# Performance work log

Measured on AMD Instinct MI355X. Metric: run time of the kernel, lower is better.

## Reference

```python
import jax, jax.numpy as jnp
import numpy as np

N = 512          # num_satellites
STATE_DIM = 6    # pos(3) + vel(3)
OBJ_DIM = 58
F = STATE_DIM + OBJ_DIM          # node feature dim = 64
HID = (128, 64, 32)
EDGE_IN = 2 * F + 1              # sender + receiver + distance
NODE_IN = F + HID[-1]            # node feats + aggregated messages


def _linear_init(key, d_in, d_out):
    kw, _ = jax.random.split(key)
    w = jax.random.normal(kw, (d_in, d_out), jnp.float32) / np.sqrt(d_in).astype(np.float32)
    b = jnp.zeros((d_out,), jnp.float32)
    return w, b


def setup_inputs() -> dict:
    key = jax.random.key(0)
    ks = jax.random.split(key, 12)
    ew0, eb0 = _linear_init(ks[0], EDGE_IN, HID[0])
    ew1, eb1 = _linear_init(ks[1], HID[0], HID[1])
    ew2, eb2 = _linear_init(ks[2], HID[1], HID[2])
    nw0, nb0 = _linear_init(ks[3], NODE_IN, HID[0])
    nw1, nb1 = _linear_init(ks[4], HID[0], HID[1])
    nw2, nb2 = _linear_init(ks[5], HID[1], HID[2])
    nwo, nbo = _linear_init(ks[6], HID[2], F)   # residual projection back to F
    rw, rb = _linear_init(ks[7], F, 3)          # control readout
    states = jax.random.normal(ks[8], (N, STATE_DIM), jnp.float32)
    objectives = jax.random.normal(ks[9], (OBJ_DIM,), jnp.float32)
    return dict(states=states, objectives=objectives,
                ew0=ew0, eb0=eb0, ew1=ew1, eb1=eb1, ew2=ew2, eb2=eb2,
                nw0=nw0, nb0=nb0, nw1=nw1, nb1=nb1, nw2=nw2, nb2=nb2,
                nwo=nwo, nbo=nbo, rw=rw, rb=rb,
                num_message_passing=3)


def _edge_index(n):
    ii, jj = np.meshgrid(np.arange(n), np.arange(n), indexing='ij')
    m = ii != jj
    return jnp.asarray(ii[m]), jnp.asarray(jj[m])  # sender i, receiver j; E = n*(n-1)


def reference(states, objectives, ew0, eb0, ew1, eb1, ew2, eb2,
              nw0, nb0, nw1, nb1, nw2, nb2, nwo, nbo, rw, rb,
              num_message_passing):
    n = states.shape[0]
    snd, rcv = _edge_index(n)
    # node features: state concat broadcast objectives -> [N, F]
    nf = jnp.concatenate(
        [states, jnp.broadcast_to(objectives, (n, objectives.shape[0]))], axis=-1)
    # distances from raw states (constant across iterations): [E, 1]
    rel = states[rcv, :3] - states[snd, :3]
    dist = jnp.linalg.norm(rel, axis=-1, keepdims=True)
    relu = jax.nn.relu
    for _ in range(num_message_passing):
        # edge MLP over all E edges: [E, 2F+1] -> [E, 32]
        x = jnp.concatenate([nf[snd], nf[rcv], dist], axis=-1)
        h = relu(x @ ew0 + eb0)
        h = relu(h @ ew1 + eb1)
        msg = relu(h @ ew2 + eb2)
        # sum-aggregate incoming messages at receiver j: [N, 32]
        agg = jax.ops.segment_sum(msg, rcv, num_segments=n)
        # node MLP + residual: [N, F+32] -> [N, F]
        y = jnp.concatenate([nf, agg], axis=-1)
        h = relu(y @ nw0 + nb0)
        h = relu(h @ nw1 + nb1)
        h = relu(h @ nw2 + nb2)
        nf = nf + h @ nwo + nbo
    # control readout: [N, 3]
    return nf @ rw + rb
```

## Files before the change

### kernel.cpp

```cpp
#include <hip/hip_runtime.h>
#include <math.h>

#define NSAT 512
#define FDIM 64
#define H0D  128
#define H1D  64
#define H2D  32
#define KP1  68

#define WS_NF    0
#define WS_PRES  (WS_NF   + NSAT * FDIM)
#define WS_PRER  (WS_PRES + NSAT * H0D)
#define WS_AGG   (WS_PRER + NSAT * H0D)
#define WS_WT    (WS_AGG  + 4 * NSAT * H2D)

using short8_t = __attribute__((ext_vector_type(8))) short;
using short4_t = __attribute__((ext_vector_type(4))) short;
using int4_t   = __attribute__((ext_vector_type(4))) int;
using int2_t   = __attribute__((ext_vector_type(2))) int;
using floatx4  = __attribute__((ext_vector_type(4))) float;
using floatx16 = __attribute__((ext_vector_type(16))) float;

__device__ __forceinline__ void split_ru(float x, short& hi, short& lo) {
    unsigned u = __builtin_bit_cast(unsigned, x);
    unsigned hb = (u + 0x8000u) >> 16;
    hi = (short)hb;
    float r = x - __builtin_bit_cast(float, hb << 16);
    lo = (short)((__builtin_bit_cast(unsigned, r) + 0x8000u) >> 16);
}

__device__ __forceinline__ void split8_pk(const float* __restrict__ v,
                                          short8_t& bh, short8_t& bl) {
    unsigned t[8]; unsigned ru[8];
    #pragma unroll
    for (int e = 0; e < 8; ++e) {
        unsigned u = __builtin_bit_cast(unsigned, v[e]);
        t[e] = u + 0x8000u;
        float r = v[e] - __builtin_bit_cast(float, t[e] & 0xffff0000u);
        ru[e] = __builtin_bit_cast(unsigned, r);
    }
    int4_t hv, lv;
    #pragma unroll
    for (int p = 0; p < 4; ++p) {
        hv[p] = (int)__builtin_amdgcn_perm(t[2*p+1],  t[2*p],  0x07060302u);
        lv[p] = (int)__builtin_amdgcn_perm(ru[2*p+1], ru[2*p], 0x07060302u);
    }
    bh = __builtin_bit_cast(short8_t, hv);
    bl = __builtin_bit_cast(short8_t, lv);
}

__device__ __forceinline__ void split4_pk(const float* __restrict__ v,
                                          short4_t& h, short4_t& l) {
    unsigned t[4]; unsigned ru[4];
    #pragma unroll
    for (int e = 0; e < 4; ++e) {
        unsigned u = __builtin_bit_cast(unsigned, v[e]);
        t[e] = u + 0x8000u;
        float r = v[e] - __builtin_bit_cast(float, t[e] & 0xffff0000u);
        ru[e] = __builtin_bit_cast(unsigned, r);
    }
    int2_t hv, lv;
    #pragma unroll
    for (int p = 0; p < 2; ++p) {
        hv[p] = (int)__builtin_amdgcn_perm(t[2*p+1],  t[2*p],  0x07060302u);
        lv[p] = (int)__builtin_amdgcn_perm(ru[2*p+1], ru[2*p], 0x07060302u);
    }
    h = __builtin_bit_cast(short4_t, hv);
    l = __builtin_bit_cast(short4_t, lv);
}

__device__ __forceinline__ float dot8(const float* __restrict__ x,
                                      const float* __restrict__ w,
                                      int n, int stride, int col, float bias) {
    float s[8] = {bias, 0.f, 0.f, 0.f, 0.f, 0.f, 0.f, 0.f};
    #pragma unroll
    for (int f = 0; f < 8; ++f) {
        for (int q = f; q < n; q += 8)
            ;
    }
    return s[0];
}

__device__ __forceinline__ void compute_pre(const float* __restrict__ nfl,
                                            const float* __restrict__ ew0,
                                            const float* __restrict__ eb0,
                                            int i, int t,
                                            float* __restrict__ preSA,
                                            float* __restrict__ preR) {
    if (t < H0D) {
        int k = t;
        float s[8] = {0.f, 0.f, 0.f, 0.f, 0.f, 0.f, 0.f, 0.f};
        #pragma unroll
        for (int f = 0; f < FDIM; f += 8) {
            #pragma unroll
            for (int e = 0; e < 8; ++e)
                s[e] = fmaf(nfl[f + e], ew0[(f + e) * H0D + k], s[e]);
        }
        float r = ((s[0] + s[1]) + (s[2] + s[3])) + ((s[4] + s[5]) + (s[6] + s[7]));
        int kk = (k >> 3) & 7, lhi = k >> 6, j = k & 7;
        preSA[((i >> 5) * 8 + kk) * 512 + (lhi * 32 + (i & 31)) * 8 + j] = r;
    } else {
        int k = t - H0D;
        float s[8] = {eb0[k], 0.f, 0.f, 0.f, 0.f, 0.f, 0.f, 0.f};
        #pragma unroll
        for (int f = 0; f < FDIM; f += 8) {
            #pragma unroll
            for (int e = 0; e < 8; ++e)
                s[e] = fmaf(nfl[f + e], ew0[(FDIM + f + e) * H0D + k], s[e]);
        }
        preR[i * H0D + k] =
            ((s[0] + s[1]) + (s[2] + s[3])) + ((s[4] + s[5]) + (s[6] + s[7]));
    }
}

__global__ void setup_kernel(const float* __restrict__ states,
                             const float* __restrict__ objectives,
                             const float* __restrict__ ew0,
                             const float* __restrict__ eb0,
                             const float* __restrict__ ew1,
                             const float* __restrict__ ew2,
                             float* __restrict__ nf,
                             float* __restrict__ preSA,
                             float* __restrict__ preR,
                             short* __restrict__ w1A_hi,
                             short* __restrict__ w1A_lo,
                             short* __restrict__ w2t_hi,
                             short* __restrict__ w2t_lo) {
    __shared__ float nfl[FDIM];
    int b = blockIdx.x, t = threadIdx.x;
    if (b < NSAT) {
        if (t < FDIM) {
            float v = (t < 6) ? states[b * 6 + t] : objectives[t - 6];
            nfl[t] = v;
            nf[b * FDIM + t] = v;
        }
        __syncthreads();
        compute_pre(nfl, ew0, eb0, b, t, preSA, preR);
    } else {
        int e = (b - NSAT) * 256 + t;
        if (e < H1D * H0D) {
            int j  = e & 7;
            int l  = (e >> 3) & 63;
            int kk = (e >> 9) & 7;
            int mh = e >> 12;
            int m = mh * 32 + (l & 31);
            int k = (l >> 5) * 64 + kk * 8 + j;
            short hi, lo; split_ru(ew1[k * H1D + m], hi, lo);
            w1A_hi[e] = hi; w1A_lo[e] = lo;
        } else if (e < H1D * H0D + H2D * H1D) {
            int e2 = e - H1D * H0D;
            int c = e2 >> 6, k = e2 & 63;
            short hi, lo; split_ru(ew2[k * H2D + c], hi, lo);
            w2t_hi[e2] = hi; w2t_lo[e2] = lo;
        }
    }
}

__global__ __launch_bounds__(256)
void edge_agg_kernel(const float* __restrict__ states,
                     const float* __restrict__ preSA,
                     const float* __restrict__ preR,
                     const float* __restrict__ ew0,
                     const float* __restrict__ eb1,
                     const float* __restrict__ eb2,
                     const short* __restrict__ w1A_hi,
                     const short* __restrict__ w1A_lo,
                     const short* __restrict__ w2t_hi,
                     const short* __restrict__ w2t_lo,
                     float* __restrict__ aggP) {
    __shared__ __align__(16) short h1_hi[128 * KP1];
    __shared__ __align__(16) short h1_lo[128 * KP1];
    __shared__ __align__(16) float preR_l[H0D];
    __shared__ __align__(16) float wd_l[H0D];
    __shared__ __align__(16) float eb1_l[H1D];
    __shared__ float eb2_l[H2D];
    __shared__ __align__(16) float red_l[4 * H2D];

    int t = threadIdx.x, b = blockIdx.x;
    int j = b >> 2, g = b & 3;
    int w = t >> 6, lane = t & 63;
    int lhi = lane >> 5, llo = lane & 31;

    if (t < H0D) preR_l[t] = preR[j * H0D + t];
    else         wd_l[t - H0D] = ew0[H0D * H0D + (t - H0D)];
    if (t < 64)      eb1_l[t] = eb1[t];
    else if (t < 96) eb2_l[t - 64] = eb2[t - 64];
    __syncthreads();

    int s_loc = w * 32 + llo;
    int s_glb = g * 128 + s_loc;
    float dx = states[s_glb * 6 + 0] - states[j * 6 + 0];
    float dy = states[s_glb * 6 + 1] - states[j * 6 + 1];
    float dz = states[s_glb * 6 + 2] - states[j * 6 + 2];
    float d = sqrtf(dx * dx + dy * dy + dz * dz);

    const float* pS = preSA + (size_t)((g * 4 + w) * 8) * 512 + lane * 8;
    const short* pAh0 = w1A_hi + lane * 8;
    const short* pAl0 = w1A_lo + lane * 8;

    floatx16 accA, accB;
    #pragma unroll
    for (int r = 0; r < 16; ++r) { accA[r] = 0.f; accB[r] = 0.f; }

    #pragma unroll
    for (int kk = 0; kk < 8; ++kk) {
        float4 a0 = *(const float4*)(pS + kk * 512);
        float4 a1 = *(const float4*)(pS + kk * 512 + 4);
        int kb = lhi * 64 + kk * 8;
        float4 r0 = *(const float4*)&preR_l[kb];
        float4 r1 = *(const float4*)&preR_l[kb + 4];
        float4 q0 = *(const float4*)&wd_l[kb];
        float4 q1 = *(const float4*)&wd_l[kb + 4];
        float v[8];
        v[0] = fmaxf(a0.x + fmaf(d, q0.x, r0.x), 0.f);
        v[1] = fmaxf(a0.y + fmaf(d, q0.y, r0.y), 0.f);
        v[2] = fmaxf(a0.z + fmaf(d, q0.z, r0.z), 0.f);
        v[3] = fmaxf(a0.w + fmaf(d, q0.w, r0.w), 0.f);
        v[4] = fmaxf(a1.x + fmaf(d, q1.x, r1.x), 0.f);
        v[5] = fmaxf(a1.y + fmaf(d, q1.y, r1.y), 0.f);
        v[6] = fmaxf(a1.z + fmaf(d, q1.z, r1.z), 0.f);
        v[7] = fmaxf(a1.w + fmaf(d, q1.w, r1.w), 0.f);
        short8_t bh, bl;
        split8_pk(v, bh, bl);
        short8_t ah0 = *(const short8_t*)(pAh0 + kk * 512);
        short8_t al0 = *(const short8_t*)(pAl0 + kk * 512);
        short8_t ah1 = *(const short8_t*)(pAh0 + 4096 + kk * 512);
        short8_t al1 = *(const short8_t*)(pAl0 + 4096 + kk * 512);
        accA = __builtin_amdgcn_mfma_f32_32x32x16_bf16(ah0, bh, accA, 0, 0, 0);
        accA = __builtin_amdgcn_mfma_f32_32x32x16_bf16(ah0, bl, accA, 0, 0, 0);
        accA = __builtin_amdgcn_mfma_f32_32x32x16_bf16(al0, bh, accA, 0, 0, 0);
        accB = __builtin_amdgcn_mfma_f32_32x32x16_bf16(ah1, bh, accB, 0, 0, 0);
        accB = __builtin_amdgcn_mfma_f32_32x32x16_bf16(ah1, bl, accB, 0, 0, 0);
        accB = __builtin_amdgcn_mfma_f32_32x32x16_bf16(al1, bh, accB, 0, 0, 0);
    }

    {
        int s1 = s_loc;
        #pragma unroll
        for (int mh = 0; mh < 2; ++mh) {
            #pragma unroll
            for (int q = 0; q < 4; ++q) {
                int m0 = mh * 32 + q * 8 + lhi * 4;
                float vv[4];
                #pragma unroll
                for (int r = 0; r < 4; ++r) {
                    float c = mh ? accB[q * 4 + r] : accA[q * 4 + r];
                    vv[r] = fmaxf(c + eb1_l[m0 + r], 0.f);
                }
                short4_t ph, pl;
                split4_pk(vv, ph, pl);
                *(short4_t*)&h1_hi[s1 * KP1 + m0] = ph;
                *(short4_t*)&h1_lo[s1 * KP1 + m0] = pl;
            }
        }
    }

    int lq = lane >> 4, l15 = lane & 15;
    int sA = w * 32 + l15, sB = sA + 16;
    floatx4 aA0, aA1, aB0, aB1;
    #pragma unroll
    for (int r = 0; r < 4; ++r) { aA0[r]=0.f; aA1[r]=0.f; aB0[r]=0.f; aB1[r]=0.f; }
    const short* pA2h0 = w2t_hi + l15 * H1D + lq * 8;
    const short* pA2l0 = w2t_lo + l15 * H1D + lq * 8;
    const short* pA2h1 = w2t_hi + (16 + l15) * H1D + lq * 8;
    const short* pA2l1 = w2t_lo + (16 + l15) * H1D + lq * 8;
    int boA = sA * KP1 + lq * 8, boB = sB * KP1 + lq * 8;
    #pragma unroll
    for (int kk = 0; kk < 2; ++kk) {
        short4_t b0, b1, c0, c1;
        b0 = *(const short4_t*)&h1_hi[boA + kk * 32];
        b1 = *(const short4_t*)&h1_hi[boA + kk * 32 + 4];
        c0 = *(const short4_t*)&h1_lo[boA + kk * 32];
        c1 = *(const short4_t*)&h1_lo[boA + kk * 32 + 4];
        short8_t bhA = __builtin_shufflevector(b0, b1, 0,1,2,3,4,5,6,7);
        short8_t blA = __builtin_shufflevector(c0, c1, 0,1,2,3,4,5,6,7);
        b0 = *(const short4_t*)&h1_hi[boB + kk * 32];
        b1 = *(const short4_t*)&h1_hi[boB + kk * 32 + 4];
        c0 = *(const short4_t*)&h1_lo[boB + kk * 32];
        c1 = *(const short4_t*)&h1_lo[boB + kk * 32 + 4];
        short8_t bhB = __builtin_shufflevector(b0, b1, 0,1,2,3,4,5,6,7);
        short8_t blB = __builtin_shufflevector(c0, c1, 0,1,2,3,4,5,6,7);
        short8_t a0h = *(const short8_t*)(pA2h0 + kk * 32);
        short8_t a0l = *(const short8_t*)(pA2l0 + kk * 32);
        short8_t a1h = *(const short8_t*)(pA2h1 + kk * 32);
        short8_t a1l = *(const short8_t*)(pA2l1 + kk * 32);
        aA0 = __builtin_amdgcn_mfma_f32_16x16x32_bf16(a0h, bhA, aA0, 0, 0, 0);
        aA0 = __builtin_amdgcn_mfma_f32_16x16x32_bf16(a0h, blA, aA0, 0, 0, 0);
        aA0 = __builtin_amdgcn_mfma_f32_16x16x32_bf16(a0l, bhA, aA0, 0, 0, 0);
        aA1 = __builtin_amdgcn_mfma_f32_16x16x32_bf16(a1h, bhA, aA1, 0, 0, 0);
        aA1 = __builtin_amdgcn_mfma_f32_16x16x32_bf16(a1h, blA, aA1, 0, 0, 0);
        aA1 = __builtin_amdgcn_mfma_f32_16x16x32_bf16(a1l, bhA, aA1, 0, 0, 0);
        aB0 = __builtin_amdgcn_mfma_f32_16x16x32_bf16(a0h, bhB, aB0, 0, 0, 0);
        aB0 = __builtin_amdgcn_mfma_f32_16x16x32_bf16(a0h, blB, aB0, 0, 0, 0);
        aB0 = __builtin_amdgcn_mfma_f32_16x16x32_bf16(a0l, bhB, aB0, 0, 0, 0);
        aB1 = __builtin_amdgcn_mfma_f32_16x16x32_bf16(a1h, bhB, aB1, 0, 0, 0);
        aB1 = __builtin_amdgcn_mfma_f32_16x16x32_bf16(a1h, blB, aB1, 0, 0, 0);
        aB1 = __builtin_amdgcn_mfma_f32_16x16x32_bf16(a1l, bhB, aB1, 0, 0, 0);
    }

    {
        bool selfA = (g * 128 + sA == j);
        bool selfB = (g * 128 + sB == j);
        float red[8];
        #pragma unroll
        for (int r = 0; r < 4; ++r) {
            float vA = fmaxf(aA0[r] + eb2_l[lq * 4 + r], 0.f);
            float vB = fmaxf(aB0[r] + eb2_l[lq * 4 + r], 0.f);
            if (selfA) vA = 0.f;
            if (selfB) vB = 0.f;
            float v = vA + vB;
            v += __shfl_xor(v, 1, 64); v += __shfl_xor(v, 2, 64);
            v += __shfl_xor(v, 4, 64); v += __shfl_xor(v, 8, 64);
            red[r] = v;
        }
        #pragma unroll
        for (int r = 0; r < 4; ++r) {
            float vA = fmaxf(aA1[r] + eb2_l[16 + lq * 4 + r], 0.f);
            float vB = fmaxf(aB1[r] + eb2_l[16 + lq * 4 + r], 0.f);
            if (selfA) vA = 0.f;
            if (selfB) vB = 0.f;
            float v = vA + vB;
            v += __shfl_xor(v, 1, 64); v += __shfl_xor(v, 2, 64);
            v += __shfl_xor(v, 4, 64); v += __shfl_xor(v, 8, 64);
            red[4 + r] = v;
        }
        if (l15 == 0) {
            *(float4*)&red_l[w * H2D + lq * 4] =
                make_float4(red[0], red[1], red[2], red[3]);
            *(float4*)&red_l[w * H2D + 16 + lq * 4] =
                make_float4(red[4], red[5], red[6], red[7]);
        }
    }
    __syncthreads();
    if (t < H2D) {
        float s = red_l[t] + red_l[H2D + t] + red_l[2*H2D + t] + red_l[3*H2D + t];
        aggP[(g * NSAT + j) * H2D + t] = s;
    }
}

__global__ __launch_bounds__(256)
void node_fused_kernel(const float* __restrict__ aggP,
                       const float* __restrict__ nw0, const float* __restrict__ nb0,
                       const float* __restrict__ nw1, const float* __restrict__ nb1,
                       const float* __restrict__ nw2, const float* __restrict__ nb2,
                       const float* __restrict__ nwo, const float* __restrict__ nbo,
                       const float* __restrict__ ew0, const float* __restrict__ eb0,
                       const float* __restrict__ rw,  const float* __restrict__ rb,
                       float* __restrict__ nf,
                       float* __restrict__ preSA,
                       float* __restrict__ preR,
                       float* __restrict__ out,
                       int final_iter) {
    __shared__ float y[96];
    __shared__ float hA[H0D];
    __shared__ float hB[H1D];
    __shared__ float hC[H2D];
    __shared__ float nfl[FDIM];
    int i = blockIdx.x, t = threadIdx.x;
    if (t < FDIM) y[t] = nf[i * FDIM + t];
    else if (t < 96) {
        int c = t - FDIM;
        float s = 0.f;
        #pragma unroll
        for (int g = 0; g < 4; ++g) s += aggP[(g * NSAT + i) * H2D + c];
        y[t] = s;
    }
    __syncthreads();
    if (t < H0D) {
        float s[8] = {nb0[t], 0.f, 0.f, 0.f, 0.f, 0.f, 0.f, 0.f};
        #pragma unroll
        for (int f = 0; f < 96; f += 8) {
            #pragma unroll
            for (int e = 0; e < 8; ++e)
                s[e] = fmaf(y[f + e], nw0[(f + e) * H0D + t], s[e]);
        }
        hA[t] = fmaxf(((s[0] + s[1]) + (s[2] + s[3])) +
                      ((s[4] + s[5]) + (s[6] + s[7])), 0.f);
    }
    __syncthreads();
    if (t < H1D) {
        float s[8] = {nb1[t], 0.f, 0.f, 0.f, 0.f, 0.f, 0.f, 0.f};
        #pragma unroll
        for (int k = 0; k < H0D; k += 8) {
            #pragma unroll
            for (int e = 0; e < 8; ++e)
                s[e] = fmaf(hA[k + e], nw1[(k + e) * H1D + t], s[e]);
        }
        hB[t] = fmaxf(((s[0] + s[1]) + (s[2] + s[3])) +
                      ((s[4] + s[5]) + (s[6] + s[7])), 0.f);
    }
    __syncthreads();
    if (t < H2D) {
        float s[8] = {nb2[t], 0.f, 0.f, 0.f, 0.f, 0.f, 0.f, 0.f};
        #pragma unroll
        for (int m = 0; m < H1D; m += 8) {
            #pragma unroll
            for (int e = 0; e < 8; ++e)
                s[e] = fmaf(hB[m + e], nw2[(m + e) * H2D + t], s[e]);
        }
        hC[t] = fmaxf(((s[0] + s[1]) + (s[2] + s[3])) +
                      ((s[4] + s[5]) + (s[6] + s[7])), 0.f);
    }
    __syncthreads();
    if (t < FDIM) {
        float s[8] = {nbo[t], 0.f, 0.f, 0.f, 0.f, 0.f, 0.f, 0.f};
        #pragma unroll
        for (int c = 0; c < H2D; c += 8) {
            #pragma unroll
            for (int e = 0; e < 8; ++e)
                s[e] = fmaf(hC[c + e], nwo[(c + e) * FDIM + t], s[e]);
        }
        float v = y[t] + (((s[0] + s[1]) + (s[2] + s[3])) +
                          ((s[4] + s[5]) + (s[6] + s[7])));
        nfl[t] = v;
        if (!final_iter) nf[i * FDIM + t] = v;
    }
    __syncthreads();
    if (final_iter) {
        if (t < 3) {
            float s[8] = {rb[t], 0.f, 0.f, 0.f, 0.f, 0.f, 0.f, 0.f};
            #pragma unroll
            for (int f = 0; f < FDIM; f += 8) {
                #pragma unroll
                for (int e = 0; e < 8; ++e)
                    s[e] = fmaf(nfl[f + e], rw[(f + e) * 3 + t], s[e]);
            }
            out[i * 3 + t] = ((s[0] + s[1]) + (s[2] + s[3])) +
                             ((s[4] + s[5]) + (s[6] + s[7]));
        }
    } else {
        compute_pre(nfl, ew0, eb0, i, t, preSA, preR);
    }
}

extern "C" void kernel_launch(void* const* d_in, const int* in_sizes, int n_in,
                              void* d_out, int out_size, void* d_ws, size_t ws_size,
                              hipStream_t stream) {
    const float* states     = (const float*)d_in[0];
    const float* objectives = (const float*)d_in[1];
    const float* ew0 = (const float*)d_in[2];
    const float* eb0 = (const float*)d_in[3];
    const float* ew1 = (const float*)d_in[4];
    const float* eb1 = (const float*)d_in[5];
    const float* ew2 = (const float*)d_in[6];
    const float* eb2 = (const float*)d_in[7];
    const float* nw0 = (const float*)d_in[8];
    const float* nb0 = (const float*)d_in[9];
    const float* nw1 = (const float*)d_in[10];
    const float* nb1 = (const float*)d_in[11];
    const float* nw2 = (const float*)d_in[12];
    const float* nb2 = (const float*)d_in[13];
    const float* nwo = (const float*)d_in[14];
    const float* nbo = (const float*)d_in[15];
    const float* rw  = (const float*)d_in[16];
    const float* rb  = (const float*)d_in[17];
    float* out = (float*)d_out;
    float* ws  = (float*)d_ws;

    float* nf    = ws + WS_NF;
    float* preSA = ws + WS_PRES;
    float* preR  = ws + WS_PRER;
    float* aggP  = ws + WS_AGG;
    short* w1A_hi = (short*)(ws + WS_WT);
    short* w1A_lo = w1A_hi + H1D * H0D;
    short* w2t_hi = w1A_lo + H1D * H0D;
    short* w2t_lo = w2t_hi + H2D * H1D;

    setup_kernel<<<NSAT + 40, 256, 0, stream>>>(states, objectives, ew0, eb0,
                                                ew1, ew2, nf, preSA, preR,
                                                w1A_hi, w1A_lo, w2t_hi, w2t_lo);
    for (int it = 0; it < 3; ++it) {
        edge_agg_kernel<<<4 * NSAT, 256, 0, stream>>>(states, preSA, preR, ew0,
                                                      eb1, eb2, w1A_hi, w1A_lo,
                                                      w2t_hi, w2t_lo, aggP);
        node_fused_kernel<<<NSAT, 256, 0, stream>>>(aggP, nw0, nb0, nw1, nb1,
                                                    nw2, nb2, nwo, nbo,
                                                    ew0, eb0, rw, rb,
                                                    nf, preSA, preR, out,
                                                    (it == 2) ? 1 : 0);
    }
}
```

Baseline: 183.1 us.

## Halve edge-kernel grid with two sender chunks per block; split node MLP across threads

The edge aggregation kernel now launches two blocks per receiver instead of four, and each block loops over two 128-sender chunks. It accumulates partial sums in a register, which halves the aggP partials the node kernel has to read and sum. The node kernel spreads each small dense layer across all 256 threads by splitting the K dimension, then reduces the partials through shared memory instead of leaving most threads idle. The cost is fewer blocks in the edge kernel, so less parallelism and latency hiding, plus extra barriers per chunk and per layer. A dead helper function is removed.

```diff
diff --git a/kernel.cpp b/kernel.cpp
--- a/kernel.cpp
+++ b/kernel.cpp
@@ -12,7 +12,7 @@
 #define WS_PRES  (WS_NF   + NSAT * FDIM)
 #define WS_PRER  (WS_PRES + NSAT * H0D)
 #define WS_AGG   (WS_PRER + NSAT * H0D)
-#define WS_WT    (WS_AGG  + 4 * NSAT * H2D)
+#define WS_WT    (WS_AGG  + 2 * NSAT * H2D)
 
 using short8_t = __attribute__((ext_vector_type(8))) short;
 using short4_t = __attribute__((ext_vector_type(4))) short;
@@ -67,18 +67,6 @@
     }
     h = __builtin_bit_cast(short4_t, hv);
     l = __builtin_bit_cast(short4_t, lv);
-}
-
-__device__ __forceinline__ float dot8(const float* __restrict__ x,
-                                      const float* __restrict__ w,
-                                      int n, int stride, int col, float bias) {
-    float s[8] = {bias, 0.f, 0.f, 0.f, 0.f, 0.f, 0.f, 0.f};
-    #pragma unroll
-    for (int f = 0; f < 8; ++f) {
-        for (int q = f; q < n; q += 8)
-            ;
-    }
-    return s[0];
 }
 
 __device__ __forceinline__ void compute_pre(const float* __restrict__ nfl,
@@ -177,7 +165,7 @@
     __shared__ __align__(16) float red_l[4 * H2D];
 
     int t = threadIdx.x, b = blockIdx.x;
-    int j = b >> 2, g = b & 3;
+    int j = b >> 1, gg = b & 1;
     int w = t >> 6, lane = t & 63;
     int lhi = lane >> 5, llo = lane & 31;
 
@@ -187,155 +175,162 @@
     else if (t < 96) eb2_l[t - 64] = eb2[t - 64];
     __syncthreads();
 
-    int s_loc = w * 32 + llo;
-    int s_glb = g * 128 + s_loc;
-    float dx = states[s_glb * 6 + 0] - states[j * 6 + 0];
-    float dy = states[s_glb * 6 + 1] - states[j * 6 + 1];
-    float dz = states[s_glb * 6 + 2] - states[j * 6 + 2];
-    float d = sqrtf(dx * dx + dy * dy + dz * dz);
-
-    const float* pS = preSA + (size_t)((g * 4 + w) * 8) * 512 + lane * 8;
-    const short* pAh0 = w1A_hi + lane * 8;
-    const short* pAl0 = w1A_lo + lane * 8;
-
-    floatx16 accA, accB;
-    #pragma unroll
-    for (int r = 0; r < 16; ++r) { accA[r] = 0.f; accB[r] = 0.f; }
-
-    #pragma unroll
-    for (int kk = 0; kk < 8; ++kk) {
-        float4 a0 = *(const float4*)(pS + kk * 512);
-        float4 a1 = *(const float4*)(pS + kk * 512 + 4);
-        int kb = lhi * 64 + kk * 8;
-        float4 r0 = *(const float4*)&preR_l[kb];
-        float4 r1 = *(const float4*)&preR_l[kb + 4];
-        float4 q0 = *(const float4*)&wd_l[kb];
-        float4 q1 = *(const float4*)&wd_l[kb + 4];
-        float v[8];
-        v[0] = fmaxf(a0.x + fmaf(d, q0.x, r0.x), 0.f);
-        v[1] = fmaxf(a0.y + fmaf(d, q0.y, r0.y), 0.f);
-        v[2] = fmaxf(a0.z + fmaf(d, q0.z, r0.z), 0.f);
-        v[3] = fmaxf(a0.w + fmaf(d, q0.w, r0.w), 0.f);
-        v[4] = fmaxf(a1.x + fmaf(d, q1.x, r1.x), 0.f);
-        v[5] = fmaxf(a1.y + fmaf(d, q1.y, r1.y), 0.f);
-        v[6] = fmaxf(a1.z + fmaf(d, q1.z, r1.z), 0.f);
-        v[7] = fmaxf(a1.w + fmaf(d, q1.w, r1.w), 0.f);
-        short8_t bh, bl;
-        split8_pk(v, bh, bl);
-        short8_t ah0 = *(const short8_t*)(pAh0 + kk * 512);
-        short8_t al0 = *(const short8_t*)(pAl0 + kk * 512);
-        short8_t ah1 = *(const short8_t*)(pAh0 + 4096 + kk * 512);
-        short8_t al1 = *(const short8_t*)(pAl0 + 4096 + kk * 512);
-        accA = __builtin_amdgcn_mfma_f32_32x32x16_bf16(ah0, bh, accA, 0, 0, 0);
-        accA = __builtin_amdgcn_mfma_f32_32x32x16_bf16(ah0, bl, accA, 0, 0, 0);
-        accA = __builtin_amdgcn_mfma_f32_32x32x16_bf16(al0, bh, accA, 0, 0, 0);
-        accB = __builtin_amdgcn_mfma_f32_32x32x16_bf16(ah1, bh, accB, 0, 0, 0);
-        accB = __builtin_amdgcn_mfma_f32_32x32x16_bf16(ah1, bl, accB, 0, 0, 0);
-        accB = __builtin_amdgcn_mfma_f32_32x32x16_bf16(al1, bh, accB, 0, 0, 0);
-    }
-
-    {
-        int s1 = s_loc;
-        #pragma unroll
-        for (int mh = 0; mh < 2; ++mh) {
-            #pragma unroll
-            for (int q = 0; q < 4; ++q) {
-                int m0 = mh * 32 + q * 8 + lhi * 4;
-                float vv[4];
+    float jx = states[j * 6 + 0], jy = states[j * 6 + 1], jz = states[j * 6 + 2];
+    int lq = lane >> 4, l15 = lane & 15;
+    float aggLoc = 0.f;
+
+    #pragma unroll 1
+    for (int c = 0; c < 2; ++c) {
+        int s_loc = w * 32 + llo;
+        int s_glb = gg * 256 + c * 128 + s_loc;
+        float dx = states[s_glb * 6 + 0] - jx;
+        float dy = states[s_glb * 6 + 1] - jy;
+        float dz = states[s_glb * 6 + 2] - jz;
+        float d = sqrtf(dx * dx + dy * dy + dz * dz);
+
+        const float* pS = preSA +
+            (size_t)((gg * 8 + c * 4 + w) * 8) * 512 + lane * 8;
+        const short* pAh0 = w1A_hi + lane * 8;
+        const short* pAl0 = w1A_lo + lane * 8;
+
+        floatx16 accA, accB;
+        #pragma unroll
+        for (int r = 0; r < 16; ++r) { accA[r] = 0.f; accB[r] = 0.f; }
+
+        #pragma unroll
+        for (int kk = 0; kk < 8; ++kk) {
+            float4 a0 = *(const float4*)(pS + kk * 512);
+            float4 a1 = *(const float4*)(pS + kk * 512 + 4);
+            int kb = lhi * 64 + kk * 8;
+            float4 r0 = *(const float4*)&preR_l[kb];
+            float4 r1 = *(const float4*)&preR_l[kb + 4];
+            float4 q0 = *(const float4*)&wd_l[kb];
+            float4 q1 = *(const float4*)&wd_l[kb + 4];
+            float v[8];
+            v[0] = fmaxf(a0.x + fmaf(d, q0.x, r0.x), 0.f);
+            v[1] = fmaxf(a0.y + fmaf(d, q0.y, r0.y), 0.f);
+            v[2] = fmaxf(a0.z + fmaf(d, q0.z, r0.z), 0.f);
+            v[3] = fmaxf(a0.w + fmaf(d, q0.w, r0.w), 0.f);
+            v[4] = fmaxf(a1.x + fmaf(d, q1.x, r1.x), 0.f);
+            v[5] = fmaxf(a1.y + fmaf(d, q1.y, r1.y), 0.f);
+            v[6] = fmaxf(a1.z + fmaf(d, q1.z, r1.z), 0.f);
+            v[7] = fmaxf(a1.w + fmaf(d, q1.w, r1.w), 0.f);
+            short8_t bh, bl;
+            split8_pk(v, bh, bl);
+            short8_t ah0 = *(const short8_t*)(pAh0 + kk * 512);
+            short8_t al0 = *(const short8_t*)(pAl0 + kk * 512);
+            short8_t ah1 = *(const short8_t*)(pAh0 + 4096 + kk * 512);
+            short8_t al1 = *(const short8_t*)(pAl0 + 4096 + kk * 512);
+            accA = __builtin_amdgcn_mfma_f32_32x32x16_bf16(ah0, bh, accA, 0, 0, 0);
+            accA = __builtin_amdgcn_mfma_f32_32x32x16_bf16(ah0, bl, accA, 0, 0, 0);
+            accA = __builtin_amdgcn_mfma_f32_32x32x16_bf16(al0, bh, accA, 0, 0, 0);
+            accB = __builtin_amdgcn_mfma_f32_32x32x16_bf16(ah1, bh, accB, 0, 0, 0);
+            accB = __builtin_amdgcn_mfma_f32_32x32x16_bf16(ah1, bl, accB, 0, 0, 0);
+            accB = __builtin_amdgcn_mfma_f32_32x32x16_bf16(al1, bh, accB, 0, 0, 0);
+        }
+
+        {
+            int s1 = s_loc;
+            #pragma unroll
+            for (int mh = 0; mh < 2; ++mh) {
                 #pragma unroll
-                for (int r = 0; r < 4; ++r) {
-                    float c = mh ? accB[q * 4 + r] : accA[q * 4 + r];
-                    vv[r] = fmaxf(c + eb1_l[m0 + r], 0.f);
+                for (int q = 0; q < 4; ++q) {
+                    int m0 = mh * 32 + q * 8 + lhi * 4;
+                    float vv[4];
+                    #pragma unroll
+                    for (int r = 0; r < 4; ++r) {
+                        float cc = mh ? accB[q * 4 + r] : accA[q * 4 + r];
+                        vv[r] = fmaxf(cc + eb1_l[m0 + r], 0.f);
+                    }
+                    short4_t ph, pl;
+                    split4_pk(vv, ph, pl);
+                    *(short4_t*)&h1_hi[s1 * KP1 + m0] = ph;
+                    *(short4_t*)&h1_lo[s1 * KP1 + m0] = pl;
                 }
-                short4_t ph, pl;
-                split4_pk(vv, ph, pl);
-                *(short4_t*)&h1_hi[s1 * KP1 + m0] = ph;
-                *(short4_t*)&h1_lo[s1 * KP1 + m0] = pl;
             }
         }
-    }
-
-    int lq = lane >> 4, l15 = lane & 15;
-    int sA = w * 32 + l15, sB = sA + 16;
-    floatx4 aA0, aA1, aB0, aB1;
-    #pragma unroll
-    for (int r = 0; r < 4; ++r) { aA0[r]=0.f; aA1[r]=0.f; aB0[r]=0.f; aB1[r]=0.f; }
-    const short* pA2h0 = w2t_hi + l15 * H1D + lq * 8;
-    const short* pA2l0 = w2t_lo + l15 * H1D + lq * 8;
-    const short* pA2h1 = w2t_hi + (16 + l15) * H1D + lq * 8;
-    const short* pA2l1 = w2t_lo + (16 + l15) * H1D + lq * 8;
-    int boA = sA * KP1 + lq * 8, boB = sB * KP1 + lq * 8;
-    #pragma unroll
-    for (int kk = 0; kk < 2; ++kk) {
-        short4_t b0, b1, c0, c1;
-        b0 = *(const short4_t*)&h1_hi[boA + kk * 32];
-        b1 = *(const short4_t*)&h1_hi[boA + kk * 32 + 4];
-        c0 = *(const short4_t*)&h1_lo[boA + kk * 32];
-        c1 = *(const short4_t*)&h1_lo[boA + kk * 32 + 4];
-        short8_t bhA = __builtin_shufflevector(b0, b1, 0,1,2,3,4,5,6,7);
-        short8_t blA = __builtin_shufflevector(c0, c1, 0,1,2,3,4,5,6,7);
-        b0 = *(const short4_t*)&h1_hi[boB + kk * 32];
-        b1 = *(const short4_t*)&h1_hi[boB + kk * 32 + 4];
-        c0 = *(const short4_t*)&h1_lo[boB + kk * 32];
-        c1 = *(const short4_t*)&h1_lo[boB + kk * 32 + 4];
-        short8_t bhB = __builtin_shufflevector(b0, b1, 0,1,2,3,4,5,6,7);
-        short8_t blB = __builtin_shufflevector(c0, c1, 0,1,2,3,4,5,6,7);
-        short8_t a0h = *(const short8_t*)(pA2h0 + kk * 32);
-        short8_t a0l = *(const short8_t*)(pA2l0 + kk * 32);
-        short8_t a1h = *(const short8_t*)(pA2h1 + kk * 32);
-        short8_t a1l = *(const short8_t*)(pA2l1 + kk * 32);
-        aA0 = __builtin_amdgcn_mfma_f32_16x16x32_bf16(a0h, bhA, aA0, 0, 0, 0);
-        aA0 = __builtin_amdgcn_mfma_f32_16x16x32_bf16(a0h, blA, aA0, 0, 0, 0);
-        aA0 = __builtin_amdgcn_mfma_f32_16x16x32_bf16(a0l, bhA, aA0, 0, 0, 0);
-        aA1 = __builtin_amdgcn_mfma_f32_16x16x32_bf16(a1h, bhA, aA1, 0, 0, 0);
-        aA1 = __builtin_amdgcn_mfma_f32_16x16x32_bf16(a1h, blA, aA1, 0, 0, 0);
-        aA1 = __builtin_amdgcn_mfma_f32_16x16x32_bf16(a1l, bhA, aA1, 0, 0, 0);
-        aB0 = __builtin_amdgcn_mfma_f32_16x16x32_bf16(a0h, bhB, aB0, 0, 0, 0);
-        aB0 = __builtin_amdgcn_mfma_f32_16x16x32_bf16(a0h, blB, aB0, 0, 0, 0);
-        aB0 = __builtin_amdgcn_mfma_f32_16x16x32_bf16(a0l, bhB, aB0, 0, 0, 0);
-        aB1 = __builtin_amdgcn_mfma_f32_16x16x32_bf16(a1h, bhB, aB1, 0, 0, 0);
-        aB1 = __builtin_amdgcn_mfma_f32_16x16x32_bf16(a1h, blB, aB1, 0, 0, 0);
-        aB1 = __builtin_amdgcn_mfma_f32_16x16x32_bf16(a1l, bhB, aB1, 0, 0, 0);
-    }
-
-    {
-        bool selfA = (g * 128 + sA == j);
-        bool selfB = (g * 128 + sB == j);
-        float red[8];
-        #pragma unroll
-        for (int r = 0; r < 4; ++r) {
-            float vA = fmaxf(aA0[r] + eb2_l[lq * 4 + r], 0.f);
-            float vB = fmaxf(aB0[r] + eb2_l[lq * 4 + r], 0.f);
-            if (selfA) vA = 0.f;
-            if (selfB) vB = 0.f;
-            float v = vA + vB;
-            v += __shfl_xor(v, 1, 64); v += __shfl_xor(v, 2, 64);
-            v += __shfl_xor(v, 4, 64); v += __shfl_xor(v, 8, 64);
-            red[r] = v;
-        }
-        #pragma unroll
-        for (int r = 0; r < 4; ++r) {
-            float vA = fmaxf(aA1[r] + eb2_l[16 + lq * 4 + r], 0.f);
-            float vB = fmaxf(aB1[r] + eb2_l[16 + lq * 4 + r], 0.f);
-            if (selfA) vA = 0.f;
-            if (selfB) vB = 0.f;
-            float v = vA + vB;
-            v += __shfl_xor(v, 1, 64); v += __shfl_xor(v, 2, 64);
-            v += __shfl_xor(v, 4, 64); v += __shfl_xor(v, 8, 64);
-            red[4 + r] = v;
-        }
-        if (l15 == 0) {
-            *(float4*)&red_l[w * H2D + lq * 4] =
-                make_float4(red[0], red[1], red[2], red[3]);
-            *(float4*)&red_l[w * H2D + 16 + lq * 4] =
-                make_float4(red[4], red[5], red[6], red[7]);
-        }
-    }
-    __syncthreads();
-    if (t < H2D) {
-        float s = red_l[t] + red_l[H2D + t] + red_l[2*H2D + t] + red_l[3*H2D + t];
-        aggP[(g * NSAT + j) * H2D + t] = s;
-    }
+
+        int sA = w * 32 + l15, sB = sA + 16;
+        floatx4 aA0, aA1, aB0, aB1;
+        #pragma unroll
+        for (int r = 0; r < 4; ++r) { aA0[r]=0.f; aA1[r]=0.f; aB0[r]=0.f; aB1[r]=0.f; }
+        const short* pA2h0 = w2t_hi + l15 * H1D + lq * 8;
+        const short* pA2l0 = w2t_lo + l15 * H1D + lq * 8;
+        const short* pA2h1 = w2t_hi + (16 + l15) * H1D + lq * 8;
+        const short* pA2l1 = w2t_lo + (16 + l15) * H1D + lq * 8;
+        int boA = sA * KP1 + lq * 8, boB = sB * KP1 + lq * 8;
+        #pragma unroll
+        for (int kk = 0; kk < 2; ++kk) {
+            short4_t b0, b1, c0, c1;
+            b0 = *(const short4_t*)&h1_hi[boA + kk * 32];
+            b1 = *(const short4_t*)&h1_hi[boA + kk * 32 + 4];
+            c0 = *(const short4_t*)&h1_lo[boA + kk * 32];
+            c1 = *(const short4_t*)&h1_lo[boA + kk * 32 + 4];
+            short8_t bhA = __builtin_shufflevector(b0, b1, 0,1,2,3,4,5,6,7);
+            short8_t blA = __builtin_shufflevector(c0, c1, 0,1,2,3,4,5,6,7);
+            b0 = *(const short4_t*)&h1_hi[boB + kk * 32];
+            b1 = *(const short4_t*)&h1_hi[boB + kk * 32 + 4];
+            c0 = *(const short4_t*)&h1_lo[boB + kk * 32];
+            c1 = *(const short4_t*)&h1_lo[boB + kk * 32 + 4];
+            short8_t bhB = __builtin_shufflevector(b0, b1, 0,1,2,3,4,5,6,7);
+            short8_t blB = __builtin_shufflevector(c0, c1, 0,1,2,3,4,5,6,7);
+            short8_t a0h = *(const short8_t*)(pA2h0 + kk * 32);
+            short8_t a0l = *(const short8_t*)(pA2l0 + kk * 32);
+            short8_t a1h = *(const short8_t*)(pA2h1 + kk * 32);
+            short8_t a1l = *(const short8_t*)(pA2l1 + kk * 32);
+            aA0 = __builtin_amdgcn_mfma_f32_16x16x32_bf16(a0h, bhA, aA0, 0, 0, 0);
+            aA0 = __builtin_amdgcn_mfma_f32_16x16x32_bf16(a0h, blA, aA0, 0, 0, 0);
+            aA0 = __builtin_amdgcn_mfma_f32_16x16x32_bf16(a0l, bhA, aA0, 0, 0, 0);
+            aA1 = __builtin_amdgcn_mfma_f32_16x16x32_bf16(a1h, bhA, aA1, 0, 0, 0);
+            aA1 = __builtin_amdgcn_mfma_f32_16x16x32_bf16(a1h, blA, aA1, 0, 0, 0);
+            aA1 = __builtin_amdgcn_mfma_f32_16x16x32_bf16(a1l, bhA, aA1, 0, 0, 0);
+            aB0 = __builtin_amdgcn_mfma_f32_16x16x32_bf16(a0h, bhB, aB0, 0, 0, 0);
+            aB0 = __builtin_amdgcn_mfma_f32_16x16x32_bf16(a0h, blB, aB0, 0, 0, 0);
+            aB0 = __builtin_amdgcn_mfma_f32_16x16x32_bf16(a0l, bhB, aB0, 0, 0, 0);
+            aB1 = __builtin_amdgcn_mfma_f32_16x16x32_bf16(a1h, bhB, aB1, 0, 0, 0);
+            aB1 = __builtin_amdgcn_mfma_f32_16x16x32_bf16(a1h, blB, aB1, 0, 0, 0);
+            aB1 = __builtin_amdgcn_mfma_f32_16x16x32_bf16(a1l, bhB, aB1, 0, 0, 0);
+        }
+
+        {
+            bool selfA = (gg * 256 + c * 128 + sA == j);
+            bool selfB = (gg * 256 + c * 128 + sB == j);
+            float red[8];
+            #pragma unroll
+            for (int r = 0; r < 4; ++r) {
+                float vA = fmaxf(aA0[r] + eb2_l[lq * 4 + r], 0.f);
+                float vB = fmaxf(aB0[r] + eb2_l[lq * 4 + r], 0.f);
+                if (selfA) vA = 0.f;
+                if (selfB) vB = 0.f;
+                float v = vA + vB;
+                v += __shfl_xor(v, 1, 64); v += __shfl_xor(v, 2, 64);
+                v += __shfl_xor(v, 4, 64); v += __shfl_xor(v, 8, 64);
+                red[r] = v;
+            }
+            #pragma unroll
+            for (int r = 0; r < 4; ++r) {
+                float vA = fmaxf(aA1[r] + eb2_l[16 + lq * 4 + r], 0.f);
+                float vB = fmaxf(aB1[r] + eb2_l[16 + lq * 4 + r], 0.f);
+                if (selfA) vA = 0.f;
+                if (selfB) vB = 0.f;
+                float v = vA + vB;
+                v += __shfl_xor(v, 1, 64); v += __shfl_xor(v, 2, 64);
+                v += __shfl_xor(v, 4, 64); v += __shfl_xor(v, 8, 64);
+                red[4 + r] = v;
+            }
+            if (l15 == 0) {
+                *(float4*)&red_l[w * H2D + lq * 4] =
+                    make_float4(red[0], red[1], red[2], red[3]);
+                *(float4*)&red_l[w * H2D + 16 + lq * 4] =
+                    make_float4(red[4], red[5], red[6], red[7]);
+            }
+        }
+        __syncthreads();
+        if (t < H2D)
+            aggLoc += red_l[t] + red_l[H2D + t] + red_l[2*H2D + t] + red_l[3*H2D + t];
+        __syncthreads();
+    }
+    if (t < H2D) aggP[(gg * NSAT + j) * H2D + t] = aggLoc;
 }
 
 __global__ __launch_bounds__(256)
@@ -356,62 +351,78 @@
     __shared__ float hB[H1D];
     __shared__ float hC[H2D];
     __shared__ float nfl[FDIM];
+    __shared__ float part[256];
     int i = blockIdx.x, t = threadIdx.x;
     if (t < FDIM) y[t] = nf[i * FDIM + t];
     else if (t < 96) {
         int c = t - FDIM;
-        float s = 0.f;
-        #pragma unroll
-        for (int g = 0; g < 4; ++g) s += aggP[(g * NSAT + i) * H2D + c];
-        y[t] = s;
-    }
-    __syncthreads();
-    if (t < H0D) {
-        float s[8] = {nb0[t], 0.f, 0.f, 0.f, 0.f, 0.f, 0.f, 0.f};
-        #pragma unroll
-        for (int f = 0; f < 96; f += 8) {
+        y[t] = aggP[i * H2D + c] + aggP[(NSAT + i) * H2D + c];
+    }
+    __syncthreads();
+
+    {
+        int col = t & 127, half = t >> 7;
+        float s[8] = {half ? 0.f : nb0[col], 0.f, 0.f, 0.f, 0.f, 0.f, 0.f, 0.f};
+        int f0 = half * 48;
+        #pragma unroll
+        for (int f = 0; f < 48; f += 8) {
             #pragma unroll
             for (int e = 0; e < 8; ++e)
-                s[e] = fmaf(y[f + e], nw0[(f + e) * H0D + t], s[e]);
-        }
-        hA[t] = fmaxf(((s[0] + s[1]) + (s[2] + s[3])) +
-                      ((s[4] + s[5]) + (s[6] + s[7])), 0.f);
-    }
-    __syncthreads();
-    if (t < H1D) {
-        float s[8] = {nb1[t], 0.f, 0.f, 0.f, 0.f, 0.f, 0.f, 0.f};
-        #pragma unroll
-        for (int k = 0; k < H0D; k += 8) {
+                s[e] = fmaf(y[f0 + f + e], nw0[(f0 + f + e) * H0D + col], s[e]);
+        }
+        part[t] = ((s[0] + s[1]) + (s[2] + s[3])) + ((s[4] + s[5]) + (s[6] + s[7]));
+    }
+    __syncthreads();
+    if (t < H0D) hA[t] = fmaxf(part[t] + part[128 + t], 0.f);
+    __syncthreads();
+
+    {
+        int col = t & 63, q = t >> 6;
+        float s[8] = {q ? 0.f : nb1[col], 0.f, 0.f, 0.f, 0.f, 0.f, 0.f, 0.f};
+        int f0 = q * 32;
+        #pragma unroll
+        for (int f = 0; f < 32; f += 8) {
             #pragma unroll
             for (int e = 0; e < 8; ++e)
-                s[e] = fmaf(hA[k + e], nw1[(k + e) * H1D + t], s[e]);
-        }
-        hB[t] = fmaxf(((s[0] + s[1]) + (s[2] + s[3])) +
-                      ((s[4] + s[5]) + (s[6] + s[7])), 0.f);
+                s[e] = fmaf(hA[f0 + f + e], nw1[(f0 + f + e) * H1D + col], s[e]);
+        }
+        part[t] = ((s[0] + s[1]) + (s[2] + s[3])) + ((s[4] + s[5]) + (s[6] + s[7]));
+    }
+    __syncthreads();
+    if (t < H1D)
+        hB[t] = fmaxf(part[t] + part[64 + t] + part[128 + t] + part[192 + t], 0.f);
+    __syncthreads();
+
+    {
+        int col = t & 31, q = t >> 5;
+        float s[8];
+        #pragma unroll
+        for (int e = 0; e < 8; ++e)
+            s[e] = hB[q * 8 + e] * nw2[(q * 8 + e) * H2D + col];
+        float p = ((s[0] + s[1]) + (s[2] + s[3])) + ((s[4] + s[5]) + (s[6] + s[7]));
+        part[t] = (q == 0) ? p + nb2[col] : p;
     }
     __syncthreads();
     if (t < H2D) {
-        float s[8] = {nb2[t], 0.f, 0.f, 0.f, 0.f, 0.f, 0.f, 0.f};
-        #pragma unroll
-        for (int m = 0; m < H1D; m += 8) {
-            #pragma unroll
-            for (int e = 0; e < 8; ++e)
-                s[e] = fmaf(hB[m + e], nw2[(m + e) * H2D + t], s[e]);
-        }
-        hC[t] = fmaxf(((s[0] + s[1]) + (s[2] + s[3])) +
-                      ((s[4] + s[5]) + (s[6] + s[7])), 0.f);
+        float p = 0.f;
+        #pragma unroll
+        for (int q = 0; q < 8; ++q) p += part[q * 32 + t];
+        hC[t] = fmaxf(p, 0.f);
+    }
+    __syncthreads();
+
+    {
+        int col = t & 63, q = t >> 6;
+        float s[8];
+        #pragma unroll
+        for (int e = 0; e < 8; ++e)
+            s[e] = hC[q * 8 + e] * nwo[(q * 8 + e) * FDIM + col];
+        float p = ((s[0] + s[1]) + (s[2] + s[3])) + ((s[4] + s[5]) + (s[6] + s[7]));
+        part[t] = (q == 0) ? p + nbo[col] : p;
     }
     __syncthreads();
     if (t < FDIM) {
-        float s[8] = {nbo[t], 0.f, 0.f, 0.f, 0.f, 0.f, 0.f, 0.f};
-        #pragma unroll
-        for (int c = 0; c < H2D; c += 8) {
-            #pragma unroll
-            for (int e = 0; e < 8; ++e)
-                s[e] = fmaf(hC[c + e], nwo[(c + e) * FDIM + t], s[e]);
-        }
-        float v = y[t] + (((s[0] + s[1]) + (s[2] + s[3])) +
-                          ((s[4] + s[5]) + (s[6] + s[7])));
+        float v = y[t] + part[t] + part[64 + t] + part[128 + t] + part[192 + t];
         nfl[t] = v;
         if (!final_iter) nf[i * FDIM + t] = v;
     }
@@ -470,7 +481,7 @@
                                                 ew1, ew2, nf, preSA, preR,
                                                 w1A_hi, w1A_lo, w2t_hi, w2t_lo);
     for (int it = 0; it < 3; ++it) {
-        edge_agg_kernel<<<4 * NSAT, 256, 0, stream>>>(states, preSA, preR, ew0,
+        edge_agg_kernel<<<2 * NSAT, 256, 0, stream>>>(states, preSA, preR, ew0,
                                                       eb1, eb2, w1A_hi, w1A_lo,
                                                       w2t_hi, w2t_lo, aggP);
         node_fused_kernel<<<NSAT, 256, 0, stream>>>(aggP, nw0, nb0, nw1, nb1,
```

Result: slower. 225.2 us (+23.0%).
